# Kernel optimization log

Hardware: AMD Instinct MI355X
Metric: run time of the kernel (lower is better)

Reference implementation:

```python
import jax, jax.numpy as jnp
import numpy as np

N, E, D, H, C = 50000, 1600000, 128, 2, 32

def setup_inputs() -> dict:
    key = jax.random.key(0)
    ks = jax.random.split(key, 8)
    x = jax.random.normal(ks[0], (N, D), jnp.float32)
    edge_index = jax.random.randint(ks[1], (2, E), 0, N)
    intra_enrichment_weights = jax.random.uniform(ks[2], (E,), jnp.float32)
    W = jax.random.normal(ks[3], (D, H * C), jnp.float32) * (1.0 / np.sqrt(D))
    att_src = jax.random.normal(ks[4], (H, C), jnp.float32) * 0.1
    att_dst = jax.random.normal(ks[5], (H, C), jnp.float32) * 0.1
    bias = jnp.zeros((H * C,), jnp.float32)
    enrichment_scale = jnp.asarray(0.01, jnp.float32)
    return dict(x=x, edge_index=edge_index,
                intra_enrichment_weights=intra_enrichment_weights,
                W=W, att_src=att_src, att_dst=att_dst, bias=bias,
                enrichment_scale=enrichment_scale)

def reference(x, edge_index, intra_enrichment_weights, W, att_src, att_dst, bias, enrichment_scale):
    n = x.shape[0]
    xf = jax.nn.elu(x)                       # F.elu on input features
    h = (xf @ W).reshape(n, H, C)            # [N, heads, out]
    # GATConv default add_self_loops=True
    loop = jnp.arange(n, dtype=edge_index.dtype)
    src = jnp.concatenate([edge_index[0], loop])
    dst = jnp.concatenate([edge_index[1], loop])
    a_src = jnp.einsum('nhc,hc->nh', h, att_src)   # [N, H]
    a_dst = jnp.einsum('nhc,hc->nh', h, att_dst)
    alpha = jax.nn.leaky_relu(a_src[src] + a_dst[dst], 0.2)  # [E+N, H]
    # softmax over incoming edges per destination node
    m = jax.ops.segment_max(alpha, dst, num_segments=n)
    e = jnp.exp(alpha - m[dst])
    denom = jax.ops.segment_sum(e, dst, num_segments=n)
    p = e / denom[dst]                       # every node has a self-loop -> denom > 0
    out = jax.ops.segment_sum(h[src] * p[:, :, None], dst, num_segments=n)  # [N, H, C]
    out = out.reshape(n, H * C) + bias
    # enrichment bias (scatter-mean of per-edge weights over source nodes)
    s0 = edge_index[0]
    nw = jax.ops.segment_sum(intra_enrichment_weights, s0, num_segments=n)
    cnt = jax.ops.segment_sum(jnp.ones_like(intra_enrichment_weights), s0, num_segments=n)
    nw = nw / jnp.maximum(cnt, 1.0)
    nw = jnp.clip(nw, 0.2, 5.0)
    scale_factor = 0.1 * jax.nn.sigmoid(enrichment_scale)
    return out + scale_factor * (nw[:, None] - 1.0)
```

## Files before the change

### kernel.cpp

```cpp
#include <hip/hip_runtime.h>
#include <hip/hip_fp16.h>


typedef unsigned int u32;
typedef unsigned short u16;
typedef unsigned long long u64;

#define SLOTS 2432
#define NBMAX 800
#define EPB 2048

#define XS 136
#define CS 68

typedef __attribute__((ext_vector_type(8))) short short8;
typedef __attribute__((ext_vector_type(4))) float float4v;

__device__ __forceinline__ u16 f2bf(float f) {
    union { float f; u32 u; } v; v.f = f;
    u32 r = v.u + 0x7fffu + ((v.u >> 16) & 1u);
    return (u16)(r >> 16);
}
__device__ __forceinline__ float bf2f(u16 u) {
    union { u32 i; float f; } v; v.i = ((u32)u) << 16; return v.f;
}
__device__ __forceinline__ float bf_lo(u32 u) {
    union { u32 i; float f; } v; v.i = u << 16; return v.f;
}
__device__ __forceinline__ float bf_hi(u32 u) {
    union { u32 i; float f; } v; v.i = u & 0xFFFF0000u; return v.f;
}
__device__ __forceinline__ void bf_split(float v, short& hi, short& lo) {
    u16 h = f2bf(v);
    float hf = bf2f(h);
    hi = (short)h;
    lo = (short)f2bf(v - hf);
}
__device__ __forceinline__ u16 f2h(float f) {
    __half h = __float2half(f);
    return *(u16*)&h;
}
__device__ __forceinline__ float h2f(u16 u) {
    __half h = *(__half*)&u;
    return __half2float(h);
}

__global__ __launch_bounds__(256) void k_node(
    const float* __restrict__ x, const float* __restrict__ Wm,
    const float* __restrict__ att_s, const float* __restrict__ att_d,
    u32* __restrict__ hb32, float* __restrict__ a_src, float* __restrict__ a_dst,
    int nN)
{
    __shared__ __align__(16) short Ah[64 * XS];
    __shared__ __align__(16) short Al[64 * XS];
    __shared__ __align__(16) short Bh[64 * XS];
    __shared__ __align__(16) short Bl[64 * XS];
    float* Cl = (float*)Ah;

    int t = threadIdx.x;
    int n0 = blockIdx.x * 64;

    {
        int f = t & 63, kq = t >> 6;
        for (int kk = 0; kk < 32; ++kk) {
            int k = kq * 32 + kk;
            float wv = Wm[k * 64 + f];
            short hi, lo; bf_split(wv, hi, lo);
            Bh[f * XS + k] = hi; Bl[f * XS + k] = lo;
        }
    }
    for (int j = 0; j < 8; ++j) {
        int idx = t + 256 * j;
        int r = idx >> 5, c4 = idx & 31;
        int gn = n0 + r;
        float4 xv = make_float4(0.f, 0.f, 0.f, 0.f);
        if (gn < nN) xv = ((const float4*)x)[(size_t)gn * 32 + c4];
        float e[4];
        e[0] = xv.x > 0.f ? xv.x : expm1f(xv.x);
        e[1] = xv.y > 0.f ? xv.y : expm1f(xv.y);
        e[2] = xv.z > 0.f ? xv.z : expm1f(xv.z);
        e[3] = xv.w > 0.f ? xv.w : expm1f(xv.w);
        short h4[4], l4[4];
#pragma unroll
        for (int i = 0; i < 4; ++i) bf_split(e[i], h4[i], l4[i]);
        *(short4*)&Ah[r * XS + c4 * 4] = make_short4(h4[0], h4[1], h4[2], h4[3]);
        *(short4*)&Al[r * XS + c4 * 4] = make_short4(l4[0], l4[1], l4[2], l4[3]);
    }
    __syncthreads();

    {
        int w = t >> 6, l = t & 63;
        int q = l >> 4, m = l & 15;
        int arow = w * 16 + m;
        float4v acc[4] = {};
#pragma unroll
        for (int ks = 0; ks < 4; ++ks) {
            int k0 = ks * 32 + q * 8;
            short8 ah = *(const short8*)&Ah[arow * XS + k0];
            short8 al = *(const short8*)&Al[arow * XS + k0];
#pragma unroll
            for (int nt = 0; nt < 4; ++nt) {
                short8 bh = *(const short8*)&Bh[(nt * 16 + m) * XS + k0];
                short8 bl = *(const short8*)&Bl[(nt * 16 + m) * XS + k0];
                acc[nt] = __builtin_amdgcn_mfma_f32_16x16x32_bf16(ah, bh, acc[nt], 0, 0, 0);
                acc[nt] = __builtin_amdgcn_mfma_f32_16x16x32_bf16(ah, bl, acc[nt], 0, 0, 0);
                acc[nt] = __builtin_amdgcn_mfma_f32_16x16x32_bf16(al, bh, acc[nt], 0, 0, 0);
            }
        }
        __syncthreads();
#pragma unroll
        for (int nt = 0; nt < 4; ++nt)
#pragma unroll
            for (int r = 0; r < 4; ++r)
                Cl[(w * 16 + q * 4 + r) * CS + nt * 16 + m] = acc[nt][r];
    }
    __syncthreads();

    {
        int nl = t >> 2, fq = t & 3;
        int gn = n0 + nl;
        float ps = 0.f, pd = 0.f;
        if (gn < nN) {
            float hv[16];
#pragma unroll
            for (int i = 0; i < 16; ++i) {
                int f = fq * 16 + i;
                hv[i] = Cl[nl * CS + f];
                ps = fmaf(hv[i], att_s[f], ps);
                pd = fmaf(hv[i], att_d[f], pd);
            }
#pragma unroll
            for (int i = 0; i < 8; ++i) {
                u32 pk = ((u32)f2bf(hv[2 * i + 1]) << 16) | (u32)f2bf(hv[2 * i]);
                hb32[(size_t)gn * 32 + fq * 8 + i] = pk;
            }
        }
        float ps2 = ps + __shfl_xor(ps, 1, 64);
        float pd2 = pd + __shfl_xor(pd, 1, 64);
        if (gn < nN && (fq & 1) == 0) {
            a_src[2 * gn + (fq >> 1)] = ps2;
            a_dst[2 * gn + (fq >> 1)] = pd2;
        }
    }
}

__global__ __launch_bounds__(512) void k_partA(
    const int* __restrict__ ei, const float* __restrict__ wgt,
    int* cursA, int* cursB, u32* bufA, u32* bufB, int E, int nb)
{
    __shared__ u32 arrA[EPB], arrB[EPB];
    __shared__ int cntA[NBMAX], cntB[NBMAX];
    __shared__ int lofsA[NBMAX], lofsB[NBMAX];
    __shared__ int basA[NBMAX], basB[NBMAX];

    int t = threadIdx.x;
    for (int b = t; b < nb; b += 512) { cntA[b] = 0; cntB[b] = 0; }
    __syncthreads();

    int base = blockIdx.x * EPB;
    int nv = min(EPB, E - base);
    int sv[4], dv[4]; float wv[4];
#pragma unroll
    for (int k = 0; k < 4; ++k) {
        int e = base + k * 512 + t;
        if (e < E) { sv[k] = ei[e]; dv[k] = ei[E + e]; wv[k] = wgt[e]; }
        else       { sv[k] = -1;    dv[k] = -1;        wv[k] = 0.f; }
    }
#pragma unroll
    for (int k = 0; k < 4; ++k) {
        if (dv[k] >= 0) {
            atomicAdd(&cntA[dv[k] >> 6], 1);
            atomicAdd(&cntB[sv[k] >> 6], 1);
        }
    }
    __syncthreads();
    for (int b = t; b < nb; b += 512) {
        int ca = cntA[b], cb = cntB[b];
        if (ca > 0) basA[b] = atomicAdd(&cursA[b], ca);
        if (cb > 0) basB[b] = atomicAdd(&cursB[b], cb);
    }
    __syncthreads();
    {
        int w = t >> 6, l = t & 63;
        if (w < 2) {
            const int* cnt = w ? cntB : cntA;
            int* lofs = w ? lofsB : lofsA;
            int carry = 0;
            int nch = (nb + 63) >> 6;
            for (int c = 0; c < nch; ++c) {
                int b = c * 64 + l;
                int v = (b < nb) ? cnt[b] : 0;
                int inc = v;
#pragma unroll
                for (int off = 1; off < 64; off <<= 1) {
                    int u = __shfl_up(inc, off, 64);
                    if (l >= off) inc += u;
                }
                if (b < nb) lofs[b] = carry + inc - v;
                carry += __shfl(inc, 63, 64);
            }
        }
    }
    __syncthreads();
    for (int b = t; b < nb; b += 512) { cntA[b] = 0; cntB[b] = 0; }
    __syncthreads();
#pragma unroll
    for (int k = 0; k < 4; ++k) {
        if (dv[k] >= 0) {
            int bA = dv[k] >> 6;
            int r = lofsA[bA] + atomicAdd(&cntA[bA], 1);
            arrA[r] = ((u32)dv[k] << 16) | (u32)sv[k];
            int bB = sv[k] >> 6;
            u32 wf = (u32)(wv[k] * 65535.f);
            if (wf > 0xFFFFu) wf = 0xFFFFu;
            int r2 = lofsB[bB] + atomicAdd(&cntB[bB], 1);
            arrB[r2] = ((u32)sv[k] << 16) | wf;
        }
    }
    __syncthreads();
    for (int i = t; i < nv; i += 512) {
        u32 v = arrA[i];
        int bA = v >> 22;
        int g = basA[bA] + (i - lofsA[bA]);
        if (g < SLOTS) bufA[bA * SLOTS + g] = v;
    }
    for (int i = t; i < nv; i += 512) {
        u32 v = arrB[i];
        int bB = v >> 22;
        int g = basB[bB] + (i - lofsB[bB]);
        if (g < SLOTS) bufB[bB * SLOTS + g] = v;
    }
}

__global__ __launch_bounds__(512) void k_fused(
    const u32* __restrict__ bufA, const int* __restrict__ cursA,
    const u32* __restrict__ bufB, const int* __restrict__ cursB,
    const float* __restrict__ a_src, const float* __restrict__ a_dst,
    const u32* __restrict__ hb32, const float* __restrict__ bias,
    const float* __restrict__ esc, float* __restrict__ out, int nN)
{
    __shared__ u32 stv[SLOTS];
    __shared__ u64 rec2[SLOTS];
    __shared__ int ldeg[64], lscan[64], lcur[64];
    __shared__ float add0[64], add1[64], ass0[64], ass1[64];
    __shared__ u32 usum[64];
    __shared__ float nwl[64];

    int b = blockIdx.x, t = threadIdx.x;
    int nA = cursA[b]; if (nA > SLOTS) nA = SLOTS;
    int nB = cursB[b]; if (nB > SLOTS) nB = SLOTS;

    if (t < 64) {
        ldeg[t] = 0; lcur[t] = 0; usum[t] = 0;
        int node = (b << 6) + t;
        float2 ad = make_float2(0.f, 0.f), as = make_float2(0.f, 0.f);
        if (node < nN) {
            ad = ((const float2*)a_dst)[node];
            as = ((const float2*)a_src)[node];
        }
        add0[t] = ad.x; add1[t] = ad.y; ass0[t] = as.x; ass1[t] = as.y;
    }
    __syncthreads();

    for (int i = t; i < nA; i += 512) {
        u32 v = bufA[b * SLOTS + i];
        stv[i] = v;
        atomicAdd(&ldeg[(v >> 16) & 63], 1);
    }
    for (int i = t; i < nB; i += 512) {
        u32 v = bufB[b * SLOTS + i];
        atomicAdd(&usum[(v >> 16) & 63], 0x1000000u | (v & 0xFFFFu));
    }
    __syncthreads();

    if (t < 64) lscan[t] = ldeg[t];
    __syncthreads();
    for (int off = 1; off < 64; off <<= 1) {
        int v = 0;
        if (t < 64 && t >= off) v = lscan[t - off];
        __syncthreads();
        if (t < 64) lscan[t] += v;
        __syncthreads();
    }
    if (t < 64) {
        lscan[t] -= ldeg[t];
        u32 uv = usum[t];
        float cnt = (float)(uv >> 24);
        float nw = ((float)(uv & 0xFFFFFFu) * (1.f / 65535.f)) / fmaxf(cnt, 1.f);
        nwl[t] = fminf(fmaxf(nw, 0.2f), 5.f);
    }
    __syncthreads();

    for (int i = t; i < nA; i += 512) {
        u32 v = stv[i];
        u32 s = v & 0xFFFFu;
        int dl = (v >> 16) & 63;
        float2 ap = ((const float2*)a_src)[s];
        float v0 = ap.x + add0[dl]; v0 = v0 > 0.f ? v0 : 0.2f * v0;
        float v1 = ap.y + add1[dl]; v1 = v1 > 0.f ? v1 : 0.2f * v1;
        u32 wp = ((u32)f2h(__expf(v1)) << 16) | (u32)f2h(__expf(v0));
        int pos = lscan[dl] + atomicAdd(&lcur[dl], 1);
        rec2[pos] = ((u64)wp << 32) | (s << 7);
    }
    __syncthreads();

    int lane = t & 63, w = t >> 6;
    int g = lane >> 4;
    int f4 = lane & 15;
    int headq = f4 >> 3;
    float sf = 0.1f / (1.f + __expf(-esc[0]));
    float4 bb = ((const float4*)bias)[f4];
    const char* hbp = (const char*)hb32 + (f4 << 3);

    for (int jj = 0; jj < 8; ++jj) {
        int j = w * 8 + jj;
        int node = (b << 6) + j;
        if (node >= nN) break;
        float t0 = ass0[j] + add0[j]; t0 = t0 > 0.f ? t0 : 0.2f * t0;
        float t1 = ass1[j] + add1[j]; t1 = t1 > 0.f ? t1 : 0.2f * t1;
        float es0 = __expf(t0), es1 = __expf(t1);
        float a0 = 0.f, a1 = 0.f, a2 = 0.f, a3 = 0.f;
        float ds0 = 0.f, ds1 = 0.f;
        int seg = lscan[j], len = ldeg[j];
        int it = (len + 3) >> 2;
#pragma unroll 4
        for (int k = 0; k < it; ++k) {
            int e = 4 * k + g;
            int idx = seg + (e < len ? e : len - 1);
            u64 rec = rec2[idx];
            u32 off = (u32)rec;
            u32 wp = (u32)(rec >> 32);
            float w0 = h2f((u16)wp), w1 = h2f((u16)(wp >> 16));
            if (e >= len) { w0 = 0.f; w1 = 0.f; }
            u64 hv = *(const u64*)(hbp + off);
            u32 hlo = (u32)hv, hhi = (u32)(hv >> 32);
            float wsel = headq ? w1 : w0;
            a0 = fmaf(wsel, bf_lo(hlo), a0);
            a1 = fmaf(wsel, bf_hi(hlo), a1);
            a2 = fmaf(wsel, bf_lo(hhi), a2);
            a3 = fmaf(wsel, bf_hi(hhi), a3);
            ds0 += w0; ds1 += w1;
        }
#pragma unroll
        for (int m = 16; m <= 32; m <<= 1) {
            a0 += __shfl_xor(a0, m, 64);
            a1 += __shfl_xor(a1, m, 64);
            a2 += __shfl_xor(a2, m, 64);
            a3 += __shfl_xor(a3, m, 64);
            ds0 += __shfl_xor(ds0, m, 64);
            ds1 += __shfl_xor(ds1, m, 64);
        }
        float den0 = ds0 + es0, den1 = ds1 + es1;
        u64 hs = *(const u64*)(hbp + ((size_t)node << 7));
        u32 slo = (u32)hs, shi = (u32)(hs >> 32);
        float eself = headq ? es1 : es0;
        float den = headq ? den1 : den0;
        float rden = 1.f / den;
        float en = sf * (nwl[j] - 1.f);
        float4 o;
        o.x = (a0 + eself * bf_lo(slo)) * rden + bb.x + en;
        o.y = (a1 + eself * bf_hi(slo)) * rden + bb.y + en;
        o.z = (a2 + eself * bf_lo(shi)) * rden + bb.z + en;
        o.w = (a3 + eself * bf_hi(shi)) * rden + bb.w + en;
        if (g == 0) ((float4*)out)[(size_t)node * 16 + f4] = o;
    }
}

extern "C" void kernel_launch(void* const* d_in, const int* in_sizes, int n_in,
                              void* d_out, int out_size, void* d_ws, size_t ws_size,
                              hipStream_t stream)
{
    const float* x     = (const float*)d_in[0];
    const int*   ei    = (const int*)d_in[1];
    const float* wgt   = (const float*)d_in[2];
    const float* Wm    = (const float*)d_in[3];
    const float* att_s = (const float*)d_in[4];
    const float* att_d = (const float*)d_in[5];
    const float* bias  = (const float*)d_in[6];
    const float* esc   = (const float*)d_in[7];
    float* out = (float*)d_out;

    int nN = in_sizes[0] / 128;
    int E  = in_sizes[2];
    int NB = (nN + 63) / 64;

    char* p = (char*)d_ws;
    auto alloc = [&](size_t bytes) -> char* {
        char* r = p; p += (bytes + 255) & ~(size_t)255; return r;
    };
    u32*   hb32  = (u32*)  alloc((size_t)nN * 32 * 4);
    float* a_src = (float*)alloc((size_t)nN * 2 * 4);
    float* a_dst = (float*)alloc((size_t)nN * 2 * 4);
    int*   cursA = (int*)  alloc(NBMAX * 4);
    int*   cursB = (int*)  alloc(NBMAX * 4);
    u32*   bufA  = (u32*)  alloc((size_t)NB * SLOTS * 4);
    u32*   bufB  = (u32*)  alloc((size_t)NB * SLOTS * 4);

    int nblkA = (E + EPB - 1) / EPB;

    hipMemsetAsync(cursA, 0, NBMAX * 4, stream);
    hipMemsetAsync(cursB, 0, NBMAX * 4, stream);
    k_node<<<dim3((nN + 63) / 64), dim3(256), 0, stream>>>(
        x, Wm, att_s, att_d, hb32, a_src, a_dst, nN);
    k_partA<<<dim3(nblkA), dim3(512), 0, stream>>>(
        ei, wgt, cursA, cursB, bufA, bufB, E, NB);
    k_fused<<<dim3(NB), dim3(512), 0, stream>>>(
        bufA, cursA, bufB, cursB, a_src, a_dst, hb32, bias, esc, out, nN);
}
```

Measured before the change: 200.5 us.

## Partition edges into coarse 512-node buckets and filter per 64-node block

The edge partition kernel now buckets edges by 512-node ranges (98 buckets) instead of 64-node ranges (782), which shrinks the shared-memory counter, scan and global cursor-atomic work and makes each bucket's global writes larger and more contiguous. The fused kernel now reads the whole coarse bucket (8x more data) and keeps only edges whose sub-block bits match, compacting them into shared memory with an atomic counter. This trades cheaper partitioning for 8x redundant reads and filtering in the consumer kernel. It also changes the order of edges within each block, which may alter floating-point summation order.

```diff
diff --git a/kernel.cpp b/kernel.cpp
--- a/kernel.cpp
+++ b/kernel.cpp
@@ -7,7 +7,9 @@
 typedef unsigned long long u64;
 
 #define SLOTS 2432
-#define NBMAX 800
+#define SLOTS_C 17408
+#define NBC 98
+#define NBC_MAX 128
 #define EPB 2048
 
 #define XS 136
@@ -146,15 +148,15 @@
 
 __global__ __launch_bounds__(512) void k_partA(
     const int* __restrict__ ei, const float* __restrict__ wgt,
-    int* cursA, int* cursB, u32* bufA, u32* bufB, int E, int nb)
+    int* cursA, int* cursB, u32* bufA, u32* bufB, int E, int nbc)
 {
     __shared__ u32 arrA[EPB], arrB[EPB];
-    __shared__ int cntA[NBMAX], cntB[NBMAX];
-    __shared__ int lofsA[NBMAX], lofsB[NBMAX];
-    __shared__ int basA[NBMAX], basB[NBMAX];
+    __shared__ int cntA[NBC_MAX], cntB[NBC_MAX];
+    __shared__ int lofsA[NBC_MAX], lofsB[NBC_MAX];
+    __shared__ int basA[NBC_MAX], basB[NBC_MAX];
 
     int t = threadIdx.x;
-    for (int b = t; b < nb; b += 512) { cntA[b] = 0; cntB[b] = 0; }
+    if (t < NBC_MAX) { cntA[t] = 0; cntB[t] = 0; }
     __syncthreads();
 
     int base = blockIdx.x * EPB;
@@ -169,15 +171,15 @@
 #pragma unroll
     for (int k = 0; k < 4; ++k) {
         if (dv[k] >= 0) {
-            atomicAdd(&cntA[dv[k] >> 6], 1);
-            atomicAdd(&cntB[sv[k] >> 6], 1);
-        }
-    }
-    __syncthreads();
-    for (int b = t; b < nb; b += 512) {
-        int ca = cntA[b], cb = cntB[b];
-        if (ca > 0) basA[b] = atomicAdd(&cursA[b], ca);
-        if (cb > 0) basB[b] = atomicAdd(&cursB[b], cb);
+            atomicAdd(&cntA[dv[k] >> 9], 1);
+            atomicAdd(&cntB[sv[k] >> 9], 1);
+        }
+    }
+    __syncthreads();
+    if (t < NBC_MAX) {
+        int ca = cntA[t], cb = cntB[t];
+        if (ca > 0) basA[t] = atomicAdd(&cursA[t], ca);
+        if (cb > 0) basB[t] = atomicAdd(&cursB[t], cb);
     }
     __syncthreads();
     {
@@ -186,31 +188,31 @@
             const int* cnt = w ? cntB : cntA;
             int* lofs = w ? lofsB : lofsA;
             int carry = 0;
-            int nch = (nb + 63) >> 6;
-            for (int c = 0; c < nch; ++c) {
+#pragma unroll
+            for (int c = 0; c < 2; ++c) {
                 int b = c * 64 + l;
-                int v = (b < nb) ? cnt[b] : 0;
+                int v = (b < NBC_MAX) ? cnt[b] : 0;
                 int inc = v;
 #pragma unroll
                 for (int off = 1; off < 64; off <<= 1) {
                     int u = __shfl_up(inc, off, 64);
                     if (l >= off) inc += u;
                 }
-                if (b < nb) lofs[b] = carry + inc - v;
+                if (b < NBC_MAX) lofs[b] = carry + inc - v;
                 carry += __shfl(inc, 63, 64);
             }
         }
     }
     __syncthreads();
-    for (int b = t; b < nb; b += 512) { cntA[b] = 0; cntB[b] = 0; }
+    if (t < NBC_MAX) { cntA[t] = 0; cntB[t] = 0; }
     __syncthreads();
 #pragma unroll
     for (int k = 0; k < 4; ++k) {
         if (dv[k] >= 0) {
-            int bA = dv[k] >> 6;
+            int bA = dv[k] >> 9;
             int r = lofsA[bA] + atomicAdd(&cntA[bA], 1);
             arrA[r] = ((u32)dv[k] << 16) | (u32)sv[k];
-            int bB = sv[k] >> 6;
+            int bB = sv[k] >> 9;
             u32 wf = (u32)(wv[k] * 65535.f);
             if (wf > 0xFFFFu) wf = 0xFFFFu;
             int r2 = lofsB[bB] + atomicAdd(&cntB[bB], 1);
@@ -220,15 +222,15 @@
     __syncthreads();
     for (int i = t; i < nv; i += 512) {
         u32 v = arrA[i];
-        int bA = v >> 22;
+        int bA = v >> 25;
         int g = basA[bA] + (i - lofsA[bA]);
-        if (g < SLOTS) bufA[bA * SLOTS + g] = v;
+        if (g < SLOTS_C) bufA[bA * SLOTS_C + g] = v;
     }
     for (int i = t; i < nv; i += 512) {
         u32 v = arrB[i];
-        int bB = v >> 22;
+        int bB = v >> 25;
         int g = basB[bB] + (i - lofsB[bB]);
-        if (g < SLOTS) bufB[bB * SLOTS + g] = v;
+        if (g < SLOTS_C) bufB[bB * SLOTS_C + g] = v;
     }
 }
 
@@ -245,10 +247,13 @@
     __shared__ float add0[64], add1[64], ass0[64], ass1[64];
     __shared__ u32 usum[64];
     __shared__ float nwl[64];
+    __shared__ int nm;
 
     int b = blockIdx.x, t = threadIdx.x;
-    int nA = cursA[b]; if (nA > SLOTS) nA = SLOTS;
-    int nB = cursB[b]; if (nB > SLOTS) nB = SLOTS;
+    int cb = b >> 3;
+    u32 sub = (u32)(b & 7);
+    int nAc = cursA[cb]; if (nAc > SLOTS_C) nAc = SLOTS_C;
+    int nBc = cursB[cb]; if (nBc > SLOTS_C) nBc = SLOTS_C;
 
     if (t < 64) {
         ldeg[t] = 0; lcur[t] = 0; usum[t] = 0;
@@ -260,18 +265,28 @@
         }
         add0[t] = ad.x; add1[t] = ad.y; ass0[t] = as.x; ass1[t] = as.y;
     }
-    __syncthreads();
-
-    for (int i = t; i < nA; i += 512) {
-        u32 v = bufA[b * SLOTS + i];
-        stv[i] = v;
-        atomicAdd(&ldeg[(v >> 16) & 63], 1);
-    }
-    for (int i = t; i < nB; i += 512) {
-        u32 v = bufB[b * SLOTS + i];
-        atomicAdd(&usum[(v >> 16) & 63], 0x1000000u | (v & 0xFFFFu));
-    }
-    __syncthreads();
+    if (t == 0) nm = 0;
+    __syncthreads();
+
+    const u32* bA = bufA + (size_t)cb * SLOTS_C;
+    for (int i = t; i < nAc; i += 512) {
+        u32 v = bA[i];
+        if (((v >> 22) & 7u) == sub) {
+            int pos = atomicAdd(&nm, 1);
+            if (pos < SLOTS) {
+                stv[pos] = v;
+                atomicAdd(&ldeg[(v >> 16) & 63], 1);
+            }
+        }
+    }
+    const u32* bB = bufB + (size_t)cb * SLOTS_C;
+    for (int i = t; i < nBc; i += 512) {
+        u32 v = bB[i];
+        if (((v >> 22) & 7u) == sub)
+            atomicAdd(&usum[(v >> 16) & 63], 0x1000000u | (v & 0xFFFFu));
+    }
+    __syncthreads();
+    int nA = nm; if (nA > SLOTS) nA = SLOTS;
 
     if (t < 64) lscan[t] = ldeg[t];
     __syncthreads();
@@ -382,7 +397,8 @@
 
     int nN = in_sizes[0] / 128;
     int E  = in_sizes[2];
-    int NB = (nN + 63) / 64;
+    int NB  = (nN + 63) / 64;
+    int NBc = (nN + 511) / 512;
 
     char* p = (char*)d_ws;
     auto alloc = [&](size_t bytes) -> char* {
@@ -391,19 +407,19 @@
     u32*   hb32  = (u32*)  alloc((size_t)nN * 32 * 4);
     float* a_src = (float*)alloc((size_t)nN * 2 * 4);
     float* a_dst = (float*)alloc((size_t)nN * 2 * 4);
-    int*   cursA = (int*)  alloc(NBMAX * 4);
-    int*   cursB = (int*)  alloc(NBMAX * 4);
-    u32*   bufA  = (u32*)  alloc((size_t)NB * SLOTS * 4);
-    u32*   bufB  = (u32*)  alloc((size_t)NB * SLOTS * 4);
+    int*   cursA = (int*)  alloc(NBC_MAX * 4);
+    int*   cursB = (int*)  alloc(NBC_MAX * 4);
+    u32*   bufA  = (u32*)  alloc((size_t)NBc * SLOTS_C * 4);
+    u32*   bufB  = (u32*)  alloc((size_t)NBc * SLOTS_C * 4);
 
     int nblkA = (E + EPB - 1) / EPB;
 
-    hipMemsetAsync(cursA, 0, NBMAX * 4, stream);
-    hipMemsetAsync(cursB, 0, NBMAX * 4, stream);
+    hipMemsetAsync(cursA, 0, NBC_MAX * 4, stream);
+    hipMemsetAsync(cursB, 0, NBC_MAX * 4, stream);
     k_node<<<dim3((nN + 63) / 64), dim3(256), 0, stream>>>(
         x, Wm, att_s, att_d, hb32, a_src, a_dst, nN);
     k_partA<<<dim3(nblkA), dim3(512), 0, stream>>>(
-        ei, wgt, cursA, cursB, bufA, bufB, E, NB);
+        ei, wgt, cursA, cursB, bufA, bufB, E, NBc);
     k_fused<<<dim3(NB), dim3(512), 0, stream>>>(
         bufA, cursA, bufB, cursB, a_src, a_dst, hb32, bias, esc, out, nN);
 }
```

Result: slower. 204.8 us (+2.1%).
